# Optimization experiments

Measured on AMD Instinct MI355X. Metric: run time of the kernel, lower is better.

Reference implementation:

```python
import jax, jax.numpy as jnp
import numpy as np

B, S, E, H = 4, 2048, 1024, 16
D = E // H  # head_dim = 64
SCALE = D ** -0.5
THETA = 10000.0


def _rope_tables(seq_len, head_dim):
    half = head_dim // 2
    inv_freq = 1.0 / (THETA ** (jnp.arange(half, dtype=jnp.float32) / half))
    ang = jnp.arange(seq_len, dtype=jnp.float32)[:, None] * inv_freq[None, :]  # [S, D/2]
    ang = jnp.concatenate([ang, ang], axis=-1)  # [S, D]
    return jnp.cos(ang), jnp.sin(ang)


def setup_inputs() -> dict:
    key = jax.random.key(0)
    kx, kw, ko = jax.random.split(key, 3)
    x = jax.random.normal(kx, (B, S, E), dtype=jnp.float32)
    in_proj_weight = jax.random.normal(kw, (3 * E, E), dtype=jnp.float32) * (E ** -0.5)
    in_proj_bias = jnp.zeros((3 * E,), dtype=jnp.float32)
    out_w = jax.random.normal(ko, (E, E), dtype=jnp.float32) * (E ** -0.5)
    out_b = jnp.zeros((E,), dtype=jnp.float32)
    cos, sin = _rope_tables(S, D)
    return {"x": x, "in_proj_weight": in_proj_weight, "in_proj_bias": in_proj_bias,
            "out_w": out_w, "out_b": out_b, "cos": cos, "sin": sin}


def _rotate_half(t):
    t1, t2 = jnp.split(t, 2, axis=-1)
    return jnp.concatenate([-t2, t1], axis=-1)


def reference(x, in_proj_weight, in_proj_bias, out_w, out_b, cos, sin):
    b, s, e = x.shape
    # fused QKV projection: [b, s, 3E]
    proj = x @ in_proj_weight.T + in_proj_bias
    q, k, v = jnp.split(proj, 3, axis=-1)
    # b s (h d) -> b h s d
    to_heads = lambda t: t.reshape(b, s, H, D).transpose(0, 2, 1, 3)
    q, k, v = to_heads(q), to_heads(k), to_heads(v)
    # RoPE (rotate-half) on q, k; cos/sin: [S, D] broadcast over batch/heads
    c = cos[None, None, :, :]
    sn = sin[None, None, :, :]
    q = q * c + _rotate_half(q) * sn
    k = k * c + _rotate_half(k) * sn
    # SDPA, non-causal, explicit scale = head_dim**-0.5
    scores = jnp.einsum("bhqd,bhkd->bhqk", q, k) * SCALE
    attn = jax.nn.softmax(scores, axis=-1)
    o = jnp.einsum("bhqk,bhkd->bhqd", attn, v)
    # b h s d -> b s (h d)
    o = o.transpose(0, 2, 1, 3).reshape(b, s, e)
    return o @ out_w.T + out_b
```

## Files before the change

kernel.cpp:

```cpp
#include <hip/hip_runtime.h>

#define NB 4
#define NS 2048
#define NE 1024
#define NH 16
#define ND 64
#define KVB 64

typedef unsigned short ushort_t;
typedef __attribute__((ext_vector_type(8))) short bf16x8;
typedef __attribute__((ext_vector_type(4))) float f32x4;

#define KQPRE 0.18033688011112042f

static __device__ __forceinline__ ushort_t f2bf(float f) {
    union { float f; unsigned int u; } v; v.f = f;
    unsigned int r = v.u + 0x7FFF + ((v.u >> 16) & 1);
    return (ushort_t)(r >> 16);
}
static __device__ __forceinline__ float bf2f(ushort_t b) {
    union { unsigned u; float f; } v; v.u = ((unsigned)b) << 16;
    return v.f;
}

static __device__ __forceinline__ unsigned pk_bf16(float lo, float hi) {
    unsigned r;
    asm("v_cvt_pk_bf16_f32 %0, %1, %2" : "=v"(r) : "v"(lo), "v"(hi));
    return r;
}

static __device__ __forceinline__ void gload16(const void* g, void* l) {
    __builtin_amdgcn_global_load_lds(
        (const __attribute__((address_space(1))) void*)g,
        (__attribute__((address_space(3))) void*)l,
        16, 0, 0);
}

__global__ __launch_bounds__(256)
void cvt3_f32_bf16(const float* __restrict__ x,  ushort_t* __restrict__ xb,
                   const float* __restrict__ Wi, ushort_t* __restrict__ Wib,
                   const float* __restrict__ Wo, ushort_t* __restrict__ Wob)
{
    const int blk = blockIdx.x;
    const float* src; ushort_t* dst; int i;
    if (blk < 4096)      { src = x;  dst = xb;  i = blk * 256 + threadIdx.x; }
    else if (blk < 5632) { src = Wi; dst = Wib; i = (blk - 4096) * 256 + threadIdx.x; }
    else                 { src = Wo; dst = Wob; i = (blk - 5632) * 256 + threadIdx.x; }
    const float4 a = ((const float4*)src)[i * 2];
    const float4 b = ((const float4*)src)[i * 2 + 1];
    union { ushort_t us[8]; uint4 v; } pk;
    pk.us[0] = f2bf(a.x); pk.us[1] = f2bf(a.y); pk.us[2] = f2bf(a.z); pk.us[3] = f2bf(a.w);
    pk.us[4] = f2bf(b.x); pk.us[5] = f2bf(b.y); pk.us[6] = f2bf(b.z); pk.us[7] = f2bf(b.w);
    ((uint4*)dst)[i] = pk.v;
}

template<int EPI>
__global__ __launch_bounds__(256)
void gemm_bf16(const ushort_t* __restrict__ A, const ushort_t* __restrict__ W,
               const float* __restrict__ bias, float* __restrict__ C,
               ushort_t* __restrict__ Cb, int M, int N, int K)
{
    __shared__ ushort_t As[128 * 32];
    __shared__ ushort_t Bs[128 * 32];
    const int tid  = threadIdx.x;
    const int lane = tid & 63;
    const int wid  = tid >> 6;
    const int lr   = lane & 15;
    const int lg   = lane >> 4;

    const int lin   = blockIdx.y * gridDim.x + blockIdx.x;
    const int chunk = (gridDim.x * gridDim.y) >> 3;
    const int lin2  = (lin & 7) * chunk + (lin >> 3);
    const int bx    = lin2 % gridDim.x;
    const int by    = lin2 / gridDim.x;
    const int m0 = by * 128;
    const int n0 = bx * 128;
    const int wr = wid >> 1, wc = wid & 1;

    size_t srcoff[2];
    int ldsoff[2];
#pragma unroll
    for (int p = 0; p < 2; ++p) {
        const int chnk = p * 256 + tid;
        const int row = chnk >> 2;
        const int sp  = chnk & 3;
        const int c   = sp ^ ((row >> 1) & 3);
        srcoff[p] = (size_t)row * K + c * 8;
        ldsoff[p] = (p * 256 + wid * 64) * 8;
    }
    const ushort_t* Ag = A + (size_t)m0 * K;
    const ushort_t* Wg = W + (size_t)n0 * K;

    int offa[4], offb[4];
#pragma unroll
    for (int f = 0; f < 4; ++f) {
        const int ra = wr * 64 + f * 16 + lr;
        offa[f] = ra * 32 + (lg ^ ((ra >> 1) & 3)) * 8;
        const int rb = wc * 64 + f * 16 + lr;
        offb[f] = rb * 32 + (lg ^ ((rb >> 1) & 3)) * 8;
    }

    f32x4 acc[4][4];
#pragma unroll
    for (int i = 0; i < 4; ++i)
#pragma unroll
        for (int j = 0; j < 4; ++j) acc[i][j] = (f32x4){0.f, 0.f, 0.f, 0.f};

    for (int k0 = 0; k0 < K; k0 += 32) {
        __syncthreads();
#pragma unroll
        for (int p = 0; p < 2; ++p) {
            gload16(Ag + srcoff[p] + k0, (ushort_t*)As + ldsoff[p]);
            gload16(Wg + srcoff[p] + k0, (ushort_t*)Bs + ldsoff[p]);
        }
        __syncthreads();
        bf16x8 af[4], bfr[4];
#pragma unroll
        for (int f = 0; f < 4; ++f) {
            af[f]  = *(const bf16x8*)&As[offa[f]];
            bfr[f] = *(const bf16x8*)&Bs[offb[f]];
        }
#pragma unroll
        for (int mf = 0; mf < 4; ++mf)
#pragma unroll
            for (int nf = 0; nf < 4; ++nf)
                acc[mf][nf] = __builtin_amdgcn_mfma_f32_16x16x32_bf16(
                    af[mf], bfr[nf], acc[mf][nf], 0, 0, 0);
    }

    if (EPI == 0) {
#pragma unroll
        for (int nf = 0; nf < 4; ++nf) {
            const int n = n0 + wc * 64 + nf * 16 + lr;
            const float bj = bias[n];
#pragma unroll
            for (int mf = 0; mf < 4; ++mf)
#pragma unroll
                for (int r = 0; r < 4; ++r) {
                    const int m = m0 + wr * 64 + mf * 16 + lg * 4 + r;
                    C[(size_t)m * N + n] = acc[mf][nf][r] + bj;
                }
        }
    } else {
#pragma unroll
        for (int nf = 0; nf < 4; ++nf) {
            const int n = n0 + wc * 64 + nf * 16 + lr;
            const float bj = bias[n];
            const int t = n >> 10;
            const int h = (n >> 6) & (NH - 1);
            const int d = n & (ND - 1);
#pragma unroll
            for (int mf = 0; mf < 4; ++mf)
#pragma unroll
                for (int r = 0; r < 4; ++r) {
                    const int m = m0 + wr * 64 + mf * 16 + lg * 4 + r;
                    const int b = m >> 11;
                    const int s = m & (NS - 1);
                    float v = acc[mf][nf][r] + bj;
                    if (t == 0) v *= KQPRE;
                    Cb[((size_t)((t * NB + b) * NH + h) * NS + s) * ND + d] = f2bf(v);
                }
        }
    }
}

__global__ __launch_bounds__(256)
void attn_kernel(const ushort_t* __restrict__ qkvb, ushort_t* __restrict__ obuf,
                 const float* __restrict__ cosT, const float* __restrict__ sinT)
{
    __shared__ ushort_t Ks[64 * 72];
    __shared__ ushort_t Vs[64 * 64];
    __shared__ ushort_t Ps[128 * 72];

    const int tid  = threadIdx.x;
    const int lane = tid & 63;
    const int wid  = tid >> 6;
    const int lr   = lane & 15;
    const int lg   = lane >> 4;

    const int orig = blockIdx.x;
    const int wg   = (orig & 7) * 128 + (orig >> 3);
    const int bh   = wg >> 4;
    const int b = bh >> 4, h = bh & (NH - 1);
    const int q0 = (wg & 15) * 128;

    const ushort_t* qbase = qkvb + ((size_t)((0 * NB + b) * NH + h)) * (NS * ND);
    const ushort_t* kbase = qkvb + ((size_t)((1 * NB + b) * NH + h)) * (NS * ND);
    const ushort_t* vbase = qkvb + ((size_t)((2 * NB + b) * NH + h)) * (NS * ND);

    bf16x8 onesf;
#pragma unroll
    for (int j = 0; j < 8; ++j) onesf[j] = (short)0x3F80;

    bf16x8 qf[2][2];
#pragma unroll
    for (int st = 0; st < 2; ++st) {
        const int sq = q0 + wid * 32 + st * 16 + lr;
        union { bf16x8 v; ushort_t us[8]; } qlo, qhi;
        qlo.v = *(const bf16x8*)(qbase + (size_t)sq * ND + lg * 8);
        qhi.v = *(const bf16x8*)(qbase + (size_t)sq * ND + 32 + lg * 8);
        const float4 c0 = *(const float4*)(cosT + sq * ND + lg * 8);
        const float4 c1 = *(const float4*)(cosT + sq * ND + lg * 8 + 4);
        const float4 s0 = *(const float4*)(sinT + sq * ND + lg * 8);
        const float4 s1 = *(const float4*)(sinT + sq * ND + lg * 8 + 4);
        const float cc[8] = {c0.x, c0.y, c0.z, c0.w, c1.x, c1.y, c1.z, c1.w};
        const float ss[8] = {s0.x, s0.y, s0.z, s0.w, s1.x, s1.y, s1.z, s1.w};
        union { bf16x8 v; ushort_t us[8]; } olo, ohi;
#pragma unroll
        for (int j = 0; j < 8; ++j) {
            const float x1 = bf2f(qlo.us[j]);
            const float x2 = bf2f(qhi.us[j]);
            olo.us[j] = f2bf(x1 * cc[j] - x2 * ss[j]);
            ohi.us[j] = f2bf(x2 * cc[j] + x1 * ss[j]);
        }
        qf[st][0] = olo.v;
        qf[st][1] = ohi.v;
    }

    const int sc = tid & 7;
    const int sr0 = tid >> 3;

    uint2 klo[2], khi[2];
    uint4 vrg[2];
#pragma unroll
    for (int it = 0; it < 2; ++it) {
        const int r = sr0 + it * 32;
        const ushort_t* kr = kbase + (size_t)r * ND + sc * 4;
        union { uint2 v; ushort_t us[4]; } lo, hi;
        lo.v = *(const uint2*)kr;
        hi.v = *(const uint2*)(kr + 32);
        const float4 cv = *(const float4*)(cosT + r * ND + sc * 4);
        const float4 sv = *(const float4*)(sinT + r * ND + sc * 4);
        const float cc[4] = {cv.x, cv.y, cv.z, cv.w};
        const float ss[4] = {sv.x, sv.y, sv.z, sv.w};
        float ol[4], oh[4];
#pragma unroll
        for (int j = 0; j < 4; ++j) {
            const float x1 = bf2f(lo.us[j]);
            const float x2 = bf2f(hi.us[j]);
            ol[j] = x1 * cc[j] - x2 * ss[j];
            oh[j] = x2 * cc[j] + x1 * ss[j];
        }
        klo[it] = make_uint2(pk_bf16(ol[0], ol[1]), pk_bf16(ol[2], ol[3]));
        khi[it] = make_uint2(pk_bf16(oh[0], oh[1]), pk_bf16(oh[2], oh[3]));
        vrg[it] = *(const uint4*)(vbase + r * ND + sc * 8);
    }

    f32x4 acc_o[2][4];
    f32x4 acc_l[2];
#pragma unroll
    for (int st = 0; st < 2; ++st) {
        acc_l[st] = (f32x4){0.f, 0.f, 0.f, 0.f};
#pragma unroll
        for (int dk = 0; dk < 4; ++dk) acc_o[st][dk] = (f32x4){0.f, 0.f, 0.f, 0.f};
    }

    for (int kt = 0; kt < NS; kt += KVB) {
        __syncthreads();
#pragma unroll
        for (int it = 0; it < 2; ++it) {
            const int r = sr0 + it * 32;
            *(uint2*)&Ks[r * 72 + sc * 4]      = klo[it];
            *(uint2*)&Ks[r * 72 + sc * 4 + 32] = khi[it];
            union { uint4 v; ushort_t us[8]; } pu;
            pu.v = vrg[it];
#pragma unroll
            for (int j = 0; j < 8; ++j) {
                const int sw = (j ^ sc) << 4;
                Vs[(sc * 8 + j) * 64 + ((((r * 2) ^ sw)) >> 1)] = pu.us[j];
            }
        }
        __syncthreads();
        if (kt + KVB < NS) {
#pragma unroll
            for (int it = 0; it < 2; ++it) {
                const int r = kt + KVB + sr0 + it * 32;
                const ushort_t* kr = kbase + (size_t)r * ND + sc * 4;
                union { uint2 v; ushort_t us[4]; } lo, hi;
                lo.v = *(const uint2*)kr;
                hi.v = *(const uint2*)(kr + 32);
                const float4 cv = *(const float4*)(cosT + r * ND + sc * 4);
                const float4 sv = *(const float4*)(sinT + r * ND + sc * 4);
                const float cc[4] = {cv.x, cv.y, cv.z, cv.w};
                const float ss[4] = {sv.x, sv.y, sv.z, sv.w};
                float ol[4], oh[4];
#pragma unroll
                for (int j = 0; j < 4; ++j) {
                    const float x1 = bf2f(lo.us[j]);
                    const float x2 = bf2f(hi.us[j]);
                    ol[j] = x1 * cc[j] - x2 * ss[j];
                    oh[j] = x2 * cc[j] + x1 * ss[j];
                }
                klo[it] = make_uint2(pk_bf16(ol[0], ol[1]), pk_bf16(ol[2], ol[3]));
                khi[it] = make_uint2(pk_bf16(oh[0], oh[1]), pk_bf16(oh[2], oh[3]));
                vrg[it] = *(const uint4*)(vbase + (size_t)r * ND + sc * 8);
            }
        }

        f32x4 s[2][4];
#pragma unroll
        for (int st = 0; st < 2; ++st)
#pragma unroll
            for (int kvf = 0; kvf < 4; ++kvf) s[st][kvf] = (f32x4){0.f, 0.f, 0.f, 0.f};
        __builtin_amdgcn_s_setprio(1);
#pragma unroll
        for (int kh = 0; kh < 2; ++kh)
#pragma unroll
            for (int kvf = 0; kvf < 4; ++kvf) {
                const bf16x8 kf = *(const bf16x8*)&Ks[(kvf * 16 + lr) * 72 + kh * 32 + lg * 8];
                s[0][kvf] = __builtin_amdgcn_mfma_f32_16x16x32_bf16(kf, qf[0][kh], s[0][kvf], 0, 0, 0);
                s[1][kvf] = __builtin_amdgcn_mfma_f32_16x16x32_bf16(kf, qf[1][kh], s[1][kvf], 0, 0, 0);
            }
        __builtin_amdgcn_s_setprio(0);

#pragma unroll
        for (int st = 0; st < 2; ++st) {
            const int prow = (wid * 32 + st * 16 + lr) * 72;
#pragma unroll
            for (int kvf = 0; kvf < 4; ++kvf) {
                const float p0 = __builtin_amdgcn_exp2f(s[st][kvf][0]);
                const float p1 = __builtin_amdgcn_exp2f(s[st][kvf][1]);
                const float p2 = __builtin_amdgcn_exp2f(s[st][kvf][2]);
                const float p3 = __builtin_amdgcn_exp2f(s[st][kvf][3]);
                const unsigned w01 = pk_bf16(p0, p1);
                const unsigned w23 = pk_bf16(p2, p3);
                *(uint2*)&Ps[prow + kvf * 16 + lg * 4] = make_uint2(w01, w23);
            }
        }
        asm volatile("s_waitcnt lgkmcnt(0)" ::: "memory");
        __builtin_amdgcn_sched_barrier(0);

        __builtin_amdgcn_s_setprio(1);
#pragma unroll
        for (int kh = 0; kh < 2; ++kh) {
            const bf16x8 pf0 = *(const bf16x8*)&Ps[(wid * 32 + 0  + lr) * 72 + kh * 32 + lg * 8];
            const bf16x8 pf1 = *(const bf16x8*)&Ps[(wid * 32 + 16 + lr) * 72 + kh * 32 + lg * 8];
            acc_l[0] = __builtin_amdgcn_mfma_f32_16x16x32_bf16(pf0, onesf, acc_l[0], 0, 0, 0);
            acc_l[1] = __builtin_amdgcn_mfma_f32_16x16x32_bf16(pf1, onesf, acc_l[1], 0, 0, 0);
#pragma unroll
            for (int dk = 0; dk < 4; ++dk) {
                const int d = dk * 16 + lr;
                const int sw = ((d & 7) ^ ((d >> 3) & 7)) << 4;
                const bf16x8 vf = *(const bf16x8*)&Vs[d * 64 + (((kh * 64 + lg * 16) ^ sw) >> 1)];
                acc_o[0][dk] = __builtin_amdgcn_mfma_f32_16x16x32_bf16(pf0, vf, acc_o[0][dk], 0, 0, 0);
                acc_o[1][dk] = __builtin_amdgcn_mfma_f32_16x16x32_bf16(pf1, vf, acc_o[1][dk], 0, 0, 0);
            }
        }
        __builtin_amdgcn_s_setprio(0);
    }

#pragma unroll
    for (int st = 0; st < 2; ++st) {
        float invq[4];
#pragma unroll
        for (int reg = 0; reg < 4; ++reg)
            invq[reg] = 1.0f / acc_l[st][reg];
#pragma unroll
        for (int dk = 0; dk < 4; ++dk)
#pragma unroll
            for (int reg = 0; reg < 4; ++reg) {
                const int q = q0 + wid * 32 + st * 16 + lg * 4 + reg;
                const int d = dk * 16 + lr;
                obuf[((size_t)(b * NS + q)) * NE + h * ND + d] =
                    f2bf(acc_o[st][dk][reg] * invq[reg]);
            }
    }
}

extern "C" void kernel_launch(void* const* d_in, const int* in_sizes, int n_in,
                              void* d_out, int out_size, void* d_ws, size_t ws_size,
                              hipStream_t stream)
{
    const float* x    = (const float*)d_in[0];
    const float* Win  = (const float*)d_in[1];
    const float* bin  = (const float*)d_in[2];
    const float* Wout = (const float*)d_in[3];
    const float* bout = (const float*)d_in[4];
    const float* cosT = (const float*)d_in[5];
    const float* sinT = (const float*)d_in[6];
    float* out  = (float*)d_out;

    ushort_t* qkvb  = (ushort_t*)d_ws;
    ushort_t* obufb = qkvb + (size_t)3 * NB * NH * NS * ND;
    ushort_t* xb    = obufb + (size_t)NB * NS * NE;
    ushort_t* Wib   = xb + (size_t)NB * NS * NE;
    ushort_t* Wob   = Wib + (size_t)3 * NE * NE;

    cvt3_f32_bf16<<<6144, 256, 0, stream>>>(x, xb, Win, Wib, Wout, Wob);

    gemm_bf16<1><<<dim3(3 * NE / 128, NB * NS / 128), 256, 0, stream>>>(
        xb, Wib, bin, nullptr, qkvb, NB * NS, 3 * NE, NE);
    attn_kernel<<<dim3(NB * NH * (NS / 128)), 256, 0, stream>>>(
        qkvb, obufb, cosT, sinT);
    gemm_bf16<0><<<dim3(NE / 128, NB * NS / 128), 256, 0, stream>>>(
        obufb, Wob, bout, out, nullptr, NB * NS, NE, NE);
}
```

Measured before the change: 235.5 us.

## Emit V pre-transposed from QKV GEMM to simplify attention V staging

For the V columns, the QKV projection kernel swaps the MFMA operands and writes V in a per-64-token tile layout transposed to d-major. The attention kernel can then stage V into LDS with one 16-byte store per chunk and read it with a padded row stride. Previously it scattered 8 scalar 2-byte LDS writes per chunk behind a swizzle. This adds a divergent operand-swap branch and strided bf16 scalar global stores in the GEMM epilogue. The 70-element padded stride also makes the vector LDS accesses not 16-byte aligned.

```diff
diff --git a/kernel.cpp b/kernel.cpp
--- a/kernel.cpp
+++ b/kernel.cpp
@@ -77,6 +77,8 @@
     const int n0 = bx * 128;
     const int wr = wid >> 1, wc = wid & 1;
 
+    const bool swapv = (EPI == 1) && (n0 >= 2 * NE);
+
     size_t srcoff[2];
     int ldsoff[2];
 #pragma unroll
@@ -120,12 +122,21 @@
             af[f]  = *(const bf16x8*)&As[offa[f]];
             bfr[f] = *(const bf16x8*)&Bs[offb[f]];
         }
-#pragma unroll
-        for (int mf = 0; mf < 4; ++mf)
-#pragma unroll
-            for (int nf = 0; nf < 4; ++nf)
-                acc[mf][nf] = __builtin_amdgcn_mfma_f32_16x16x32_bf16(
-                    af[mf], bfr[nf], acc[mf][nf], 0, 0, 0);
+        if (!swapv) {
+#pragma unroll
+            for (int mf = 0; mf < 4; ++mf)
+#pragma unroll
+                for (int nf = 0; nf < 4; ++nf)
+                    acc[mf][nf] = __builtin_amdgcn_mfma_f32_16x16x32_bf16(
+                        af[mf], bfr[nf], acc[mf][nf], 0, 0, 0);
+        } else {
+#pragma unroll
+            for (int mf = 0; mf < 4; ++mf)
+#pragma unroll
+                for (int nf = 0; nf < 4; ++nf)
+                    acc[mf][nf] = __builtin_amdgcn_mfma_f32_16x16x32_bf16(
+                        bfr[nf], af[mf], acc[mf][nf], 0, 0, 0);
+        }
     }
 
     if (EPI == 0) {
@@ -141,7 +152,7 @@
                     C[(size_t)m * N + n] = acc[mf][nf][r] + bj;
                 }
         }
-    } else {
+    } else if (!swapv) {
 #pragma unroll
         for (int nf = 0; nf < 4; ++nf) {
             const int n = n0 + wc * 64 + nf * 16 + lr;
@@ -161,6 +172,27 @@
                     Cb[((size_t)((t * NB + b) * NH + h) * NS + s) * ND + d] = f2bf(v);
                 }
         }
+    } else {
+        const int hv = ((n0 + wc * 64) >> 6) & (NH - 1);
+        const size_t vtoff = (size_t)2 * NB * NH * NS * ND;
+#pragma unroll
+        for (int nf = 0; nf < 4; ++nf) {
+            const float4 bv = *(const float4*)&bias[n0 + wc * 64 + nf * 16 + lg * 4];
+            const float bj[4] = {bv.x, bv.y, bv.z, bv.w};
+#pragma unroll
+            for (int mf = 0; mf < 4; ++mf) {
+                const int m = m0 + wr * 64 + mf * 16 + lr;
+                const int b = m >> 11;
+                const int s = m & (NS - 1);
+                const size_t rowbase = vtoff
+                    + (((size_t)(b * NH + hv)) * 32 + (s >> 6)) * 4096 + (s & 63);
+#pragma unroll
+                for (int r = 0; r < 4; ++r) {
+                    const int d = nf * 16 + lg * 4 + r;
+                    Cb[rowbase + (size_t)d * 64] = f2bf(acc[mf][nf][r] + bj[r]);
+                }
+            }
+        }
     }
 }
 
@@ -169,7 +201,7 @@
                  const float* __restrict__ cosT, const float* __restrict__ sinT)
 {
     __shared__ ushort_t Ks[64 * 72];
-    __shared__ ushort_t Vs[64 * 64];
+    __shared__ ushort_t Vs[64 * 70];
     __shared__ ushort_t Ps[128 * 72];
 
     const int tid  = threadIdx.x;
@@ -186,7 +218,8 @@
 
     const ushort_t* qbase = qkvb + ((size_t)((0 * NB + b) * NH + h)) * (NS * ND);
     const ushort_t* kbase = qkvb + ((size_t)((1 * NB + b) * NH + h)) * (NS * ND);
-    const ushort_t* vbase = qkvb + ((size_t)((2 * NB + b) * NH + h)) * (NS * ND);
+    const ushort_t* vbase = qkvb + (size_t)2 * NB * NH * NS * ND
+                                 + ((size_t)(b * NH + h)) * 32 * 4096;
 
     bf16x8 onesf;
 #pragma unroll
@@ -243,7 +276,7 @@
         }
         klo[it] = make_uint2(pk_bf16(ol[0], ol[1]), pk_bf16(ol[2], ol[3]));
         khi[it] = make_uint2(pk_bf16(oh[0], oh[1]), pk_bf16(oh[2], oh[3]));
-        vrg[it] = *(const uint4*)(vbase + r * ND + sc * 8);
+        vrg[it] = *(const uint4*)(vbase + (size_t)r * 64 + sc * 8);
     }
 
     f32x4 acc_o[2][4];
@@ -262,16 +295,11 @@
             const int r = sr0 + it * 32;
             *(uint2*)&Ks[r * 72 + sc * 4]      = klo[it];
             *(uint2*)&Ks[r * 72 + sc * 4 + 32] = khi[it];
-            union { uint4 v; ushort_t us[8]; } pu;
-            pu.v = vrg[it];
-#pragma unroll
-            for (int j = 0; j < 8; ++j) {
-                const int sw = (j ^ sc) << 4;
-                Vs[(sc * 8 + j) * 64 + ((((r * 2) ^ sw)) >> 1)] = pu.us[j];
-            }
+            *(uint4*)&Vs[r * 70 + sc * 8]      = vrg[it];
         }
         __syncthreads();
         if (kt + KVB < NS) {
+            const ushort_t* vtile = vbase + (size_t)((kt + KVB) >> 6) * 4096;
 #pragma unroll
             for (int it = 0; it < 2; ++it) {
                 const int r = kt + KVB + sr0 + it * 32;
@@ -293,7 +321,7 @@
                 }
                 klo[it] = make_uint2(pk_bf16(ol[0], ol[1]), pk_bf16(ol[2], ol[3]));
                 khi[it] = make_uint2(pk_bf16(oh[0], oh[1]), pk_bf16(oh[2], oh[3]));
-                vrg[it] = *(const uint4*)(vbase + (size_t)r * ND + sc * 8);
+                vrg[it] = *(const uint4*)(vtile + (size_t)(sr0 + it * 32) * 64 + sc * 8);
             }
         }
 
@@ -339,9 +367,7 @@
             acc_l[1] = __builtin_amdgcn_mfma_f32_16x16x32_bf16(pf1, onesf, acc_l[1], 0, 0, 0);
 #pragma unroll
             for (int dk = 0; dk < 4; ++dk) {
-                const int d = dk * 16 + lr;
-                const int sw = ((d & 7) ^ ((d >> 3) & 7)) << 4;
-                const bf16x8 vf = *(const bf16x8*)&Vs[d * 64 + (((kh * 64 + lg * 16) ^ sw) >> 1)];
+                const bf16x8 vf = *(const bf16x8*)&Vs[(dk * 16 + lr) * 70 + kh * 32 + lg * 8];
                 acc_o[0][dk] = __builtin_amdgcn_mfma_f32_16x16x32_bf16(pf0, vf, acc_o[0][dk], 0, 0, 0);
                 acc_o[1][dk] = __builtin_amdgcn_mfma_f32_16x16x32_bf16(pf1, vf, acc_o[1][dk], 0, 0, 0);
             }
```

Result: slower. 272.8 us (+15.8%).
